# Kernel tuning notes

Measured on AMD Instinct MI355X. Metric: run time of the kernel, lower is better.

## Reference

```python
import jax, jax.numpy as jnp
import numpy as np

D_MODEL = 512
NUM_HEADS = 8
HEAD_DIM = D_MODEL // NUM_HEADS
BATCH = 4
SEQ = 2048
ROPE_BASE = 10000.0


def rope_cos_sin(seq_len, head_dim):
    inv_freq = 1.0 / (ROPE_BASE ** (jnp.arange(0, head_dim, 2, dtype=jnp.float32) / head_dim))
    t = jnp.arange(seq_len, dtype=jnp.float32)
    freqs = jnp.outer(t, inv_freq)              # (S, head_dim/2)
    emb = jnp.concatenate([freqs, freqs], axis=-1)  # (S, head_dim)
    return jnp.cos(emb), jnp.sin(emb)


def apply_rope(x, cos, sin):
    # x: (..., S, head_dim); cos/sin: (S, head_dim)
    x1 = x[..., ::2]
    x2 = x[..., 1::2]
    ch = cos[..., ::2]
    sh = sin[..., ::2]
    r1 = x1 * ch - x2 * sh
    r2 = x1 * sh + x2 * ch
    return jnp.stack([r1, r2], axis=-1).reshape(x.shape)


def setup_inputs() -> dict:
    key = jax.random.key(0)
    ks = jax.random.split(key, 12)
    x = jax.random.normal(ks[0], (BATCH, SEQ, D_MODEL), dtype=jnp.float32)
    variate_ids = jnp.sort(jax.random.randint(ks[1], (BATCH, SEQ), 0, 8), axis=-1).astype(jnp.int64)
    mask = jnp.ones((BATCH, SEQ), dtype=jnp.float32)
    s = 1.0 / np.sqrt(D_MODEL)
    Wq = jax.random.normal(ks[2], (D_MODEL, D_MODEL), dtype=jnp.float32) * s
    bq = jnp.zeros((D_MODEL,), dtype=jnp.float32)
    Wk = jax.random.normal(ks[3], (D_MODEL, D_MODEL), dtype=jnp.float32) * s
    bk = jnp.zeros((D_MODEL,), dtype=jnp.float32)
    Wv = jax.random.normal(ks[4], (D_MODEL, D_MODEL), dtype=jnp.float32) * s
    bv = jnp.zeros((D_MODEL,), dtype=jnp.float32)
    Wo = jax.random.normal(ks[5], (D_MODEL, D_MODEL), dtype=jnp.float32) * s
    bo = jnp.zeros((D_MODEL,), dtype=jnp.float32)
    u_same = jax.random.normal(ks[6], (NUM_HEADS,), dtype=jnp.float32) * 0.1
    u_cross = jax.random.normal(ks[7], (NUM_HEADS,), dtype=jnp.float32) * 0.1
    return dict(x=x, variate_ids=variate_ids, mask=mask, Wq=Wq, bq=bq, Wk=Wk, bk=bk,
                Wv=Wv, bv=bv, Wo=Wo, bo=bo, u_same=u_same, u_cross=u_cross)


def reference(x, variate_ids, mask, Wq, bq, Wk, bk, Wv, bv, Wo, bo, u_same, u_cross):
    B, S, D = x.shape
    H, Hd = NUM_HEADS, HEAD_DIM
    scale = 1.0 / np.sqrt(Hd)

    def proj(W, b):
        return (x @ W.T + b).reshape(B, S, H, Hd).transpose(0, 2, 1, 3)  # (B,H,S,Hd)

    q = proj(Wq, bq)
    k = proj(Wk, bk)
    v = proj(Wv, bv)

    cos, sin = rope_cos_sin(S, Hd)
    q = apply_rope(q, cos, sin)
    k = apply_rope(k, cos, sin)

    scores = jnp.einsum('bhid,bhjd->bhij', q, k) * scale  # (B,H,S,S)
    same = (variate_ids[:, :, None] == variate_ids[:, None, :]).astype(jnp.float32)  # (B,S,S)
    bias = same[:, None] * u_same[None, :, None, None] + (1.0 - same)[:, None] * u_cross[None, :, None, None]
    scores = scores + bias
    scores = scores + (1.0 - mask[:, None, None, :]) * -1e9
    probs = jax.nn.softmax(scores, axis=-1)
    out = jnp.einsum('bhij,bhjd->bhid', probs, v)  # (B,H,S,Hd)
    out = out.transpose(0, 2, 1, 3).reshape(B, S, D)
    return out @ Wo.T + bo
```

## Files before the change

### kernel.cpp

```cpp
#include <hip/hip_runtime.h>
#include <hip/hip_bf16.h>

#define BATCH   4
#define SEQ     2048
#define DMODEL  512
#define NHEADS  8
#define HEADDIM 64
#define MTOT    (BATCH*SEQ)
#define NX      (MTOT*DMODEL)
#define NW      (DMODEL*DMODEL)
#define QTILE   128
#define KTILE   64
#define NKT     (SEQ/KTILE)

#define LOG2E   1.4426950408889634f
#define SCL2    0.18033688011112042f
#define SHIFT   14.426950408889634f

typedef unsigned short u16;
typedef __bf16 bf16x8 __attribute__((ext_vector_type(8)));
typedef float  f32x4  __attribute__((ext_vector_type(4)));
typedef unsigned short u16x4 __attribute__((ext_vector_type(4)));
typedef unsigned u32x2 __attribute__((ext_vector_type(2)));

#define MFMA(a,b,c) __builtin_amdgcn_mfma_f32_16x16x32_bf16(a,b,c,0,0,0)

__device__ __forceinline__ u16 f2bf(float f) {
    unsigned u = __float_as_uint(f);
    u += 0x7FFFu + ((u >> 16) & 1u);
    return (u16)(u >> 16);
}

__device__ __forceinline__ unsigned pk_bf16(float a, float b) {
    union { __hip_bfloat162 h; unsigned u; } cv;
    cv.h = __float22bfloat162_rn(make_float2(a, b));
    return cv.u;
}

__device__ __forceinline__ float qsum16(float v) {
    v += __shfl_xor(v, 1);
    v += __shfl_xor(v, 2);
    v += __shfl_xor(v, 4);
    v += __shfl_xor(v, 8);
    return v;
}

__device__ __forceinline__ void gll16(const void* g, void* l) {
    __builtin_amdgcn_global_load_lds((const __attribute__((address_space(1))) void*)g,
                                     (__attribute__((address_space(3))) void*)l, 16, 0, 0);
}
__device__ __forceinline__ void gll4(const void* g, void* l) {
    __builtin_amdgcn_global_load_lds((const __attribute__((address_space(1))) void*)g,
                                     (__attribute__((address_space(3))) void*)l, 4, 0, 0);
}

#define NCVT4 ((NX + 4*NW)/4)
__global__ __launch_bounds__(256) void cvt_rope_kernel(
    const float* __restrict__ x,
    const float* __restrict__ wq, const float* __restrict__ wk,
    const float* __restrict__ wv, const float* __restrict__ wo,
    u16* __restrict__ xbf,
    u16* __restrict__ wqbf, u16* __restrict__ wkbf,
    u16* __restrict__ wvbf, u16* __restrict__ wobf,
    float2* __restrict__ cst)
{
    int i4 = blockIdx.x * 256 + threadIdx.x;
    if (i4 < NCVT4) {
        int i = i4 * 4;
        const float* s; u16* d; int o;
        if (i < NX) { s = x; d = xbf; o = i; }
        else {
            int j = i - NX;
            int r = j >> 18;
            o = j & (NW - 1);
            s = (r == 0) ? wq : (r == 1) ? wk : (r == 2) ? wv : wo;
            d = (r == 0) ? wqbf : (r == 1) ? wkbf : (r == 2) ? wvbf : wobf;
        }
        float4 v = *(const float4*)(s + o);
        u16x4 u = { f2bf(v.x), f2bf(v.y), f2bf(v.z), f2bf(v.w) };
        *(u16x4*)(d + o) = u;
    } else {
        int r = i4 - NCVT4;
        if (r < SEQ * 32 / 4) {
            int idx = r * 4;
            int s  = idx >> 5;
            int p0 = idx & 31;
#pragma unroll
            for (int t = 0; t < 4; ++t) {
                int p = p0 + t;
                float inv = __expf(-0.5756462732485115f * (float)(p & 15));
                float ang = (float)s * inv;
                cst[idx + t] = make_float2(cosf(ang), sinf(ang));
            }
        }
    }
}

__global__ __launch_bounds__(256) void qkv_kernel(
    const u16* __restrict__ x,
    const u16* __restrict__ Wq, const float* __restrict__ bq,
    const u16* __restrict__ Wk, const float* __restrict__ bk,
    const u16* __restrict__ Wv, const float* __restrict__ bv,
    const float2* __restrict__ cst,
    u16* __restrict__ qws, u16* __restrict__ kws, u16* __restrict__ vtws)
{
    __shared__ alignas(16) u16 As[128 * 64];
    __shared__ alignas(16) u16 Bs[128 * 64];

    const int m0 = blockIdx.x * 128;
    const int n0 = blockIdx.y * 128;
    const int tid  = threadIdx.x;
    const int w    = tid >> 6;
    const int lane = tid & 63;
    const int quad = lane >> 4;
    const int l16  = lane & 15;
    const int wm = w & 1, wn = w >> 1;

    const int sec = n0 >> 9;
    const int oc0 = n0 & 511;
    const u16*   Wm = (sec == 0) ? Wq : (sec == 1 ? Wk : Wv);
    const float* bb = (sec == 0) ? bq : (sec == 1 ? bk : bv);
    const float  sgn = (l16 & 1) ? 1.0f : -1.0f;

    f32x4 acc[4][4] = {};

    for (int kb = 0; kb < 8; ++kb) {
#pragma unroll
        for (int it = 0; it < 4; ++it) {
            const int s   = it * 256 + tid;
            const int row = s >> 3;
            const int cb  = s & 7;
            const int gcol = kb * 64 + (((cb ^ (row & 7))) << 3);
            gll16(x  + (m0  + row) * 512 + gcol, &As[s * 8]);
            gll16(Wm + (oc0 + row) * 512 + gcol, &Bs[s * 8]);
        }
        __syncthreads();

#pragma unroll
        for (int ks = 0; ks < 2; ++ks) {
            bf16x8 a[4], bfr[4];
#pragma unroll
            for (int t = 0; t < 4; ++t) {
                const int arow = wm * 64 + t * 16 + l16;
                a[t]   = *(const bf16x8*)&As[arow * 64 + (((ks * 4 + quad) ^ (arow & 7)) << 3)];
                const int brow = wn * 64 + t * 16 + l16;
                bfr[t] = *(const bf16x8*)&Bs[brow * 64 + (((ks * 4 + quad) ^ (brow & 7)) << 3)];
            }
#pragma unroll
            for (int tm = 0; tm < 4; ++tm)
#pragma unroll
                for (int tn = 0; tn < 4; ++tn)
                    acc[tm][tn] = MFMA(a[tm], bfr[tn], acc[tm][tn]);
        }
        __syncthreads();
    }

#pragma unroll
    for (int tm = 0; tm < 4; ++tm) {
        const int R0 = m0 + wm * 64 + tm * 16 + quad * 4;
        const int bi = R0 >> 11;
        const int s0 = R0 & 2047;
#pragma unroll
        for (int tn = 0; tn < 4; ++tn) {
            const int col = oc0 + wn * 64 + tn * 16 + l16;
            const int hh  = col >> 6;
            const int d   = col & 63;
            const float bval = bb[col];
            const size_t hb = (size_t)(bi * NHEADS + hh) * (SEQ * HEADDIM);
            float res[4];
            if (sec < 2) {
#pragma unroll
                for (int r = 0; r < 4; ++r) {
                    float val = acc[tm][tn][r] + bval;
                    float other = __shfl_xor(val, 1);
                    float2 cs = cst[(s0 + r) * 32 + (d >> 1)];
                    res[r] = fmaf(val, cs.x, other * (sgn * cs.y));
                }
                const unsigned p01 = pk_bf16(res[0], res[1]);
                const unsigned p23 = pk_bf16(res[2], res[3]);
                u16* dp = ((sec == 0) ? qws : kws) + hb + (size_t)s0 * HEADDIM + d;
                dp[0]   = (u16)p01;  dp[64]  = (u16)(p01 >> 16);
                dp[128] = (u16)p23;  dp[192] = (u16)(p23 >> 16);
            } else {
#pragma unroll
                for (int r = 0; r < 4; ++r) res[r] = acc[tm][tn][r] + bval;
                u32x2 pv = { pk_bf16(res[0], res[1]), pk_bf16(res[2], res[3]) };
                *(u32x2*)(vtws + hb + (size_t)d * SEQ + s0) = pv;
            }
        }
    }
}

__global__ __launch_bounds__(512, 4) void attn_kernel(
    const u16* __restrict__ qws, const u16* __restrict__ kws,
    const u16* __restrict__ vtl,
    const int* __restrict__ vids, const float* __restrict__ mask,
    const float* __restrict__ u_same, const float* __restrict__ u_cross,
    u16* __restrict__ attn)
{
    __shared__ alignas(16) u16 kbuf[2][KTILE * 64];
    __shared__ alignas(16) u16 vbuf[2][KTILE * 64];
    __shared__ alignas(16) u16 pls[8][16][72];
    __shared__ int   bid[2][KTILE];
    __shared__ float bmk[2][KTILE];

    const int bh = blockIdx.y;
    const int b  = bh >> 3;
    const int h  = bh & 7;
    const int q0 = blockIdx.x * QTILE;

    const int tid  = threadIdx.x;
    const int w    = tid >> 6;
    const int lane = tid & 63;
    const int quad = lane >> 4;
    const int l16  = lane & 15;

    const float us2 = u_same[h]  * LOG2E;
    const float uc2 = u_cross[h] * LOG2E;
    const size_t tb = (size_t)bh * (SEQ * HEADDIM);

    const int qr = q0 + w * 16 + l16;
    const bf16x8 aq0 = *(const bf16x8*)(qws + tb + qr * HEADDIM + quad * 8);
    const bf16x8 aq1 = *(const bf16x8*)(qws + tb + qr * HEADDIM + 32 + quad * 8);

    int vq[4];
#pragma unroll
    for (int r = 0; r < 4; ++r)
        vq[r] = vids[b * SEQ + q0 + w * 16 + quad * 4 + r];

    float li[4] = {0.f, 0.f, 0.f, 0.f};
    f32x4 o[4] = {};

    const int srow = w * 8 + (lane >> 3);
    const int scb  = lane & 7;
    const int soff = ((scb ^ (srow & 7)) << 3);
    auto stage = [&](int kt, int nb) {
        const int k0 = kt * KTILE;
        gll16(kws + tb + (size_t)(k0 + srow) * HEADDIM + soff, &kbuf[nb][w * 512 + (lane & 7) * 8 + ((lane >> 3) & 7) * 0 + lane * 8 - lane * 8 + (srow - w * 8) * 64 + scb * 8]);
        gll16(vtl + tb + (size_t)srow * SEQ + k0 + soff,        &vbuf[nb][(srow - w * 8) * 64 + w * 512 + scb * 8]);
        if (w == 0) {
            gll4(vids + b * SEQ + k0 + lane, &bid[nb][0]);
            gll4(mask + b * SEQ + k0 + lane, &bmk[nb][0]);
        }
    };

    auto body = [&](const int cur) {
#pragma unroll
        for (int nt = 0; nt < 4; ++nt) {
            const int krow = nt * 16 + l16;
            const int r7   = krow & 7;
            const bf16x8 kb0 = *(const bf16x8*)&kbuf[cur][krow * 64 + ((quad ^ r7) << 3)];
            const bf16x8 kb1 = *(const bf16x8*)&kbuf[cur][krow * 64 + ((quad ^ r7 ^ 4) << 3)];
            f32x4 sc = {};
            sc = MFMA(aq0, kb0, sc);
            sc = MFMA(aq1, kb1, sc);
            const int   kv  = bid[cur][krow];
            const float mdl = fmaf(bmk[cur][krow], 1.4426950408889634e9f,
                                   -1.4426950408889634e9f - SHIFT);
            const float as_ = us2 + mdl;
            const float ac_ = uc2 + mdl;
            float p[4];
#pragma unroll
            for (int r = 0; r < 4; ++r) {
                const float sel = (kv == vq[r]) ? as_ : ac_;
                p[r] = exp2f(fmaf(sc[r], SCL2, sel));
                li[r] += p[r];
            }
            const unsigned p01 = pk_bf16(p[0], p[1]);
            const unsigned p23 = pk_bf16(p[2], p[3]);
            u16* pb = &pls[w][quad * 4][nt * 16 + l16];
            pb[0]       = (u16)p01;  pb[72]      = (u16)(p01 >> 16);
            pb[2 * 72]  = (u16)p23;  pb[3 * 72]  = (u16)(p23 >> 16);
        }

        const bf16x8 ap0 = *(const bf16x8*)&pls[w][l16][quad * 8];
        const bf16x8 ap1 = *(const bf16x8*)&pls[w][l16][32 + quad * 8];

#pragma unroll
        for (int nt = 0; nt < 4; ++nt) {
            const int vrow = nt * 16 + l16;
            const int r7   = vrow & 7;
            const bf16x8 vb0 = *(const bf16x8*)&vbuf[cur][vrow * 64 + ((quad ^ r7) << 3)];
            const bf16x8 vb1 = *(const bf16x8*)&vbuf[cur][vrow * 64 + ((quad ^ r7 ^ 4) << 3)];
            o[nt] = MFMA(ap0, vb0, o[nt]);
            o[nt] = MFMA(ap1, vb1, o[nt]);
        }
    };

    stage(0, 0);
    for (int kt = 0; kt < NKT; kt += 2) {
        __syncthreads();
        stage(kt + 1, 1);
        body(0);
        __syncthreads();
        if (kt + 2 < NKT) stage(kt + 2, 0);
        body(1);
    }

#pragma unroll
    for (int r = 0; r < 4; ++r) {
        const float inv = 1.0f / qsum16(li[r]);
        const int R = q0 + w * 16 + quad * 4 + r;
        const int rb = (b * SEQ + R) * DMODEL + h * HEADDIM;
#pragma unroll
        for (int nt = 0; nt < 4; ++nt)
            attn[rb + nt * 16 + l16] = f2bf(o[nt][r] * inv);
    }
}

__global__ __launch_bounds__(256) void proj_kernel(
    const u16* __restrict__ a, const u16* __restrict__ Wo,
    const float* __restrict__ bo, float* __restrict__ out)
{
    __shared__ alignas(16) u16 As[128 * 64];
    __shared__ alignas(16) u16 Bs[128 * 64];

    const int m0 = blockIdx.x * 128;
    const int n0 = blockIdx.y * 128;
    const int tid  = threadIdx.x;
    const int w    = tid >> 6;
    const int lane = tid & 63;
    const int quad = lane >> 4;
    const int l16  = lane & 15;
    const int wm = w & 1, wn = w >> 1;

    f32x4 acc[4][4] = {};

    for (int kb = 0; kb < 8; ++kb) {
#pragma unroll
        for (int it = 0; it < 4; ++it) {
            const int s   = it * 256 + tid;
            const int row = s >> 3;
            const int cb  = s & 7;
            const int gcol = kb * 64 + (((cb ^ (row & 7))) << 3);
            gll16(a  + (m0 + row) * 512 + gcol, &As[s * 8]);
            gll16(Wo + (n0 + row) * 512 + gcol, &Bs[s * 8]);
        }
        __syncthreads();

#pragma unroll
        for (int ks = 0; ks < 2; ++ks) {
            bf16x8 av[4], bv[4];
#pragma unroll
            for (int t = 0; t < 4; ++t) {
                const int arow = wm * 64 + t * 16 + l16;
                av[t] = *(const bf16x8*)&As[arow * 64 + (((ks * 4 + quad) ^ (arow & 7)) << 3)];
                const int brow = wn * 64 + t * 16 + l16;
                bv[t] = *(const bf16x8*)&Bs[brow * 64 + (((ks * 4 + quad) ^ (brow & 7)) << 3)];
            }
#pragma unroll
            for (int tm = 0; tm < 4; ++tm)
#pragma unroll
                for (int tn = 0; tn < 4; ++tn)
                    acc[tm][tn] = MFMA(av[tm], bv[tn], acc[tm][tn]);
        }
        __syncthreads();
    }

#pragma unroll
    for (int tm = 0; tm < 4; ++tm) {
#pragma unroll
        for (int tn = 0; tn < 4; ++tn) {
            const int col = n0 + wn * 64 + tn * 16 + l16;
            const float bval = bo[col];
#pragma unroll
            for (int r = 0; r < 4; ++r) {
                const int R = m0 + wm * 64 + tm * 16 + quad * 4 + r;
                out[R * 512 + col] = acc[tm][tn][r] + bval;
            }
        }
    }
}

extern "C" void kernel_launch(void* const* d_in, const int* in_sizes, int n_in,
                              void* d_out, int out_size, void* d_ws, size_t ws_size,
                              hipStream_t stream) {
    const float* x    = (const float*)d_in[0];
    const int*   vids = (const int*)d_in[1];
    const float* mask = (const float*)d_in[2];
    const float* Wq = (const float*)d_in[3];
    const float* bq = (const float*)d_in[4];
    const float* Wk = (const float*)d_in[5];
    const float* bk = (const float*)d_in[6];
    const float* Wv = (const float*)d_in[7];
    const float* bv = (const float*)d_in[8];
    const float* Wo = (const float*)d_in[9];
    const float* bo = (const float*)d_in[10];
    const float* usame  = (const float*)d_in[11];
    const float* ucross = (const float*)d_in[12];
    float* out = (float*)d_out;

    u16* xbf  = (u16*)d_ws;
    u16* wqbf = xbf + NX;
    u16* wkbf = wqbf + NW;
    u16* wvbf = wkbf + NW;
    u16* wobf = wvbf + NW;
    float2* cst = (float2*)(wobf + NW);
    u16* qws  = (u16*)(cst + SEQ * 32);
    u16* kws  = qws + (size_t)BATCH * NHEADS * SEQ * HEADDIM;
    u16* vtws = kws + (size_t)BATCH * NHEADS * SEQ * HEADDIM;
    u16* attn = xbf;

    cvt_rope_kernel<<<(NCVT4 + SEQ * 32 / 4 + 255) / 256, 256, 0, stream>>>(
        x, Wq, Wk, Wv, Wo, xbf, wqbf, wkbf, wvbf, wobf, cst);

    dim3 g1(MTOT / 128, 3 * DMODEL / 128);
    qkv_kernel<<<g1, 256, 0, stream>>>(xbf, wqbf, bq, wkbf, bk, wvbf, bv,
                                       cst, qws, kws, vtws);

    dim3 g2(SEQ / QTILE, BATCH * NHEADS);
    attn_kernel<<<g2, 512, 0, stream>>>(qws, kws, vtws, vids, mask,
                                        usame, ucross, attn);

    dim3 g3(MTOT / 128, DMODEL / 128);
    proj_kernel<<<g3, 256, 0, stream>>>(attn, wobf, bo, out);
}
```

Baseline: 207.1 us.

## Process two query subtiles per attention wave and stage V transpose through LDS

The attention kernel moves from 512 to 256 threads per block, with each wave now handling two 16-row query subtiles. K and V fragments read from shared memory are reused across both subtiles, which halves LDS reads per MFMA, at the cost of more registers per thread. Separately, the QKV kernel's V epilogue now writes the transposed tile into padded shared memory and then emits coalesced 16-byte global stores, replacing the scattered 8-byte transposed stores.

```diff
diff --git a/kernel.cpp b/kernel.cpp
--- a/kernel.cpp
+++ b/kernel.cpp
@@ -96,6 +96,7 @@
     }
 }
 
+#define TP 136
 __global__ __launch_bounds__(256) void qkv_kernel(
     const u16* __restrict__ x,
     const u16* __restrict__ Wq, const float* __restrict__ bq,
@@ -104,8 +105,9 @@
     const float2* __restrict__ cst,
     u16* __restrict__ qws, u16* __restrict__ kws, u16* __restrict__ vtws)
 {
-    __shared__ alignas(16) u16 As[128 * 64];
-    __shared__ alignas(16) u16 Bs[128 * 64];
+    __shared__ alignas(16) u16 smem[128 * TP];
+    u16* As = smem;
+    u16* Bs = smem + 8192;
 
     const int m0 = blockIdx.x * 128;
     const int n0 = blockIdx.y * 128;
@@ -155,20 +157,20 @@
         __syncthreads();
     }
 
-#pragma unroll
-    for (int tm = 0; tm < 4; ++tm) {
-        const int R0 = m0 + wm * 64 + tm * 16 + quad * 4;
-        const int bi = R0 >> 11;
-        const int s0 = R0 & 2047;
-#pragma unroll
-        for (int tn = 0; tn < 4; ++tn) {
-            const int col = oc0 + wn * 64 + tn * 16 + l16;
-            const int hh  = col >> 6;
-            const int d   = col & 63;
-            const float bval = bb[col];
-            const size_t hb = (size_t)(bi * NHEADS + hh) * (SEQ * HEADDIM);
-            float res[4];
-            if (sec < 2) {
+    if (sec < 2) {
+#pragma unroll
+        for (int tm = 0; tm < 4; ++tm) {
+            const int R0 = m0 + wm * 64 + tm * 16 + quad * 4;
+            const int bi = R0 >> 11;
+            const int s0 = R0 & 2047;
+#pragma unroll
+            for (int tn = 0; tn < 4; ++tn) {
+                const int col = oc0 + wn * 64 + tn * 16 + l16;
+                const int hh  = col >> 6;
+                const int d   = col & 63;
+                const float bval = bb[col];
+                const size_t hb = (size_t)(bi * NHEADS + hh) * (SEQ * HEADDIM);
+                float res[4];
 #pragma unroll
                 for (int r = 0; r < 4; ++r) {
                     float val = acc[tm][tn][r] + bval;
@@ -181,17 +183,40 @@
                 u16* dp = ((sec == 0) ? qws : kws) + hb + (size_t)s0 * HEADDIM + d;
                 dp[0]   = (u16)p01;  dp[64]  = (u16)(p01 >> 16);
                 dp[128] = (u16)p23;  dp[192] = (u16)(p23 >> 16);
-            } else {
-#pragma unroll
-                for (int r = 0; r < 4; ++r) res[r] = acc[tm][tn][r] + bval;
-                u32x2 pv = { pk_bf16(res[0], res[1]), pk_bf16(res[2], res[3]) };
-                *(u32x2*)(vtws + hb + (size_t)d * SEQ + s0) = pv;
-            }
-        }
-    }
-}
-
-__global__ __launch_bounds__(512, 4) void attn_kernel(
+            }
+        }
+    } else {
+#pragma unroll
+        for (int tm = 0; tm < 4; ++tm) {
+            const int row_l = wm * 64 + tm * 16 + quad * 4;
+#pragma unroll
+            for (int tn = 0; tn < 4; ++tn) {
+                const int col_l = wn * 64 + tn * 16 + l16;
+                const float bval = bb[oc0 + col_l];
+                u32x2 pv = { pk_bf16(acc[tm][tn][0] + bval, acc[tm][tn][1] + bval),
+                             pk_bf16(acc[tm][tn][2] + bval, acc[tm][tn][3] + bval) };
+                *(u32x2*)&smem[col_l * TP + row_l] = pv;
+            }
+        }
+        __syncthreads();
+        const int bi  = m0 >> 11;
+        const int sgb = m0 & 2047;
+#pragma unroll
+        for (int i = 0; i < 8; ++i) {
+            const int c    = i * 256 + tid;
+            const int col  = c >> 4;
+            const int sc8  = (c & 15) * 8;
+            const int gcol = oc0 + col;
+            const int hh   = gcol >> 6;
+            const int d    = gcol & 63;
+            u16* dst = vtws + (size_t)(bi * NHEADS + hh) * (SEQ * HEADDIM)
+                            + (size_t)d * SEQ + sgb + sc8;
+            *(bf16x8*)dst = *(const bf16x8*)&smem[col * TP + sc8];
+        }
+    }
+}
+
+__global__ __launch_bounds__(256) void attn_kernel(
     const u16* __restrict__ qws, const u16* __restrict__ kws,
     const u16* __restrict__ vtl,
     const int* __restrict__ vids, const float* __restrict__ mask,
@@ -200,7 +225,7 @@
 {
     __shared__ alignas(16) u16 kbuf[2][KTILE * 64];
     __shared__ alignas(16) u16 vbuf[2][KTILE * 64];
-    __shared__ alignas(16) u16 pls[8][16][72];
+    __shared__ alignas(16) u16 pls[4][32][72];
     __shared__ int   bid[2][KTILE];
     __shared__ float bmk[2][KTILE];
 
@@ -219,25 +244,34 @@
     const float uc2 = u_cross[h] * LOG2E;
     const size_t tb = (size_t)bh * (SEQ * HEADDIM);
 
-    const int qr = q0 + w * 16 + l16;
-    const bf16x8 aq0 = *(const bf16x8*)(qws + tb + qr * HEADDIM + quad * 8);
-    const bf16x8 aq1 = *(const bf16x8*)(qws + tb + qr * HEADDIM + 32 + quad * 8);
-
-    int vq[4];
-#pragma unroll
-    for (int r = 0; r < 4; ++r)
-        vq[r] = vids[b * SEQ + q0 + w * 16 + quad * 4 + r];
-
-    float li[4] = {0.f, 0.f, 0.f, 0.f};
-    f32x4 o[4] = {};
-
-    const int srow = w * 8 + (lane >> 3);
-    const int scb  = lane & 7;
-    const int soff = ((scb ^ (srow & 7)) << 3);
+    bf16x8 aq[2][2];
+#pragma unroll
+    for (int s = 0; s < 2; ++s) {
+        const int qr = q0 + s * 64 + w * 16 + l16;
+        aq[s][0] = *(const bf16x8*)(qws + tb + qr * HEADDIM + quad * 8);
+        aq[s][1] = *(const bf16x8*)(qws + tb + qr * HEADDIM + 32 + quad * 8);
+    }
+    int vq[2][4];
+#pragma unroll
+    for (int s = 0; s < 2; ++s)
+#pragma unroll
+        for (int r = 0; r < 4; ++r)
+            vq[s][r] = vids[b * SEQ + q0 + s * 64 + w * 16 + quad * 4 + r];
+
+    float li[2][4] = {};
+    f32x4 o[2][4] = {};
+
     auto stage = [&](int kt, int nb) {
         const int k0 = kt * KTILE;
-        gll16(kws + tb + (size_t)(k0 + srow) * HEADDIM + soff, &kbuf[nb][w * 512 + (lane & 7) * 8 + ((lane >> 3) & 7) * 0 + lane * 8 - lane * 8 + (srow - w * 8) * 64 + scb * 8]);
-        gll16(vtl + tb + (size_t)srow * SEQ + k0 + soff,        &vbuf[nb][(srow - w * 8) * 64 + w * 512 + scb * 8]);
+#pragma unroll
+        for (int i = 0; i < 2; ++i) {
+            const int srow = w * 16 + i * 8 + (lane >> 3);
+            const int scb  = lane & 7;
+            const int soff = ((scb ^ (srow & 7)) << 3);
+            const int doff = srow * 64 + scb * 8;
+            gll16(kws + tb + (size_t)(k0 + srow) * HEADDIM + soff, &kbuf[nb][doff]);
+            gll16(vtl + tb + (size_t)srow * SEQ + k0 + soff,       &vbuf[nb][doff]);
+        }
         if (w == 0) {
             gll4(vids + b * SEQ + k0 + lane, &bid[nb][0]);
             gll4(mask + b * SEQ + k0 + lane, &bmk[nb][0]);
@@ -251,30 +285,37 @@
             const int r7   = krow & 7;
             const bf16x8 kb0 = *(const bf16x8*)&kbuf[cur][krow * 64 + ((quad ^ r7) << 3)];
             const bf16x8 kb1 = *(const bf16x8*)&kbuf[cur][krow * 64 + ((quad ^ r7 ^ 4) << 3)];
-            f32x4 sc = {};
-            sc = MFMA(aq0, kb0, sc);
-            sc = MFMA(aq1, kb1, sc);
             const int   kv  = bid[cur][krow];
             const float mdl = fmaf(bmk[cur][krow], 1.4426950408889634e9f,
                                    -1.4426950408889634e9f - SHIFT);
             const float as_ = us2 + mdl;
             const float ac_ = uc2 + mdl;
-            float p[4];
-#pragma unroll
-            for (int r = 0; r < 4; ++r) {
-                const float sel = (kv == vq[r]) ? as_ : ac_;
-                p[r] = exp2f(fmaf(sc[r], SCL2, sel));
-                li[r] += p[r];
-            }
-            const unsigned p01 = pk_bf16(p[0], p[1]);
-            const unsigned p23 = pk_bf16(p[2], p[3]);
-            u16* pb = &pls[w][quad * 4][nt * 16 + l16];
-            pb[0]       = (u16)p01;  pb[72]      = (u16)(p01 >> 16);
-            pb[2 * 72]  = (u16)p23;  pb[3 * 72]  = (u16)(p23 >> 16);
-        }
-
-        const bf16x8 ap0 = *(const bf16x8*)&pls[w][l16][quad * 8];
-        const bf16x8 ap1 = *(const bf16x8*)&pls[w][l16][32 + quad * 8];
+#pragma unroll
+            for (int s = 0; s < 2; ++s) {
+                f32x4 sc = {};
+                sc = MFMA(aq[s][0], kb0, sc);
+                sc = MFMA(aq[s][1], kb1, sc);
+                float p[4];
+#pragma unroll
+                for (int r = 0; r < 4; ++r) {
+                    const float sel = (kv == vq[s][r]) ? as_ : ac_;
+                    p[r] = exp2f(fmaf(sc[r], SCL2, sel));
+                    li[s][r] += p[r];
+                }
+                const unsigned p01 = pk_bf16(p[0], p[1]);
+                const unsigned p23 = pk_bf16(p[2], p[3]);
+                u16* pb = &pls[w][s * 16 + quad * 4][nt * 16 + l16];
+                pb[0]      = (u16)p01;  pb[72]     = (u16)(p01 >> 16);
+                pb[2 * 72] = (u16)p23;  pb[3 * 72] = (u16)(p23 >> 16);
+            }
+        }
+
+        bf16x8 ap[2][2];
+#pragma unroll
+        for (int s = 0; s < 2; ++s) {
+            ap[s][0] = *(const bf16x8*)&pls[w][s * 16 + l16][quad * 8];
+            ap[s][1] = *(const bf16x8*)&pls[w][s * 16 + l16][32 + quad * 8];
+        }
 
 #pragma unroll
         for (int nt = 0; nt < 4; ++nt) {
@@ -282,8 +323,11 @@
             const int r7   = vrow & 7;
             const bf16x8 vb0 = *(const bf16x8*)&vbuf[cur][vrow * 64 + ((quad ^ r7) << 3)];
             const bf16x8 vb1 = *(const bf16x8*)&vbuf[cur][vrow * 64 + ((quad ^ r7 ^ 4) << 3)];
-            o[nt] = MFMA(ap0, vb0, o[nt]);
-            o[nt] = MFMA(ap1, vb1, o[nt]);
+#pragma unroll
+            for (int s = 0; s < 2; ++s) {
+                o[s][nt] = MFMA(ap[s][0], vb0, o[s][nt]);
+                o[s][nt] = MFMA(ap[s][1], vb1, o[s][nt]);
+            }
         }
     };
 
@@ -298,14 +342,16 @@
     }
 
 #pragma unroll
-    for (int r = 0; r < 4; ++r) {
-        const float inv = 1.0f / qsum16(li[r]);
-        const int R = q0 + w * 16 + quad * 4 + r;
-        const int rb = (b * SEQ + R) * DMODEL + h * HEADDIM;
-#pragma unroll
-        for (int nt = 0; nt < 4; ++nt)
-            attn[rb + nt * 16 + l16] = f2bf(o[nt][r] * inv);
-    }
+    for (int s = 0; s < 2; ++s)
+#pragma unroll
+        for (int r = 0; r < 4; ++r) {
+            const float inv = 1.0f / qsum16(li[s][r]);
+            const int R = q0 + s * 64 + w * 16 + quad * 4 + r;
+            const int rb = (b * SEQ + R) * DMODEL + h * HEADDIM;
+#pragma unroll
+            for (int nt = 0; nt < 4; ++nt)
+                attn[rb + nt * 16 + l16] = f2bf(o[s][nt][r] * inv);
+        }
 }
 
 __global__ __launch_bounds__(256) void proj_kernel(
@@ -409,7 +455,7 @@
                                        cst, qws, kws, vtws);
 
     dim3 g2(SEQ / QTILE, BATCH * NHEADS);
-    attn_kernel<<<g2, 512, 0, stream>>>(qws, kws, vtws, vids, mask,
+    attn_kernel<<<g2, 256, 0, stream>>>(qws, kws, vtws, vids, mask,
                                         usame, ucross, attn);
 
     dim3 g3(MTOT / 128, DMODEL / 128);
```

Measured after the change: 215.2 us. 3.9% more time.

## Stage GEMM epilogues through LDS for coalesced 16-byte global stores

Applied to the files above, without the earlier changes.

The QKV and output-projection GEMM epilogues now transpose their accumulator tiles into padded shared memory, then write to global memory with wide coalesced vector stores. This replaces the scattered 2-byte and 4-byte writes. For Q/K the MFMA operand order is swapped so each lane holds consecutive head-dim elements, which lets RoPE pairs be rotated in-register without shuffles. The cost is extra LDS traffic and barriers, and the output projection now runs its epilogue in two halves.

```diff
diff --git a/kernel.cpp b/kernel.cpp
--- a/kernel.cpp
+++ b/kernel.cpp
@@ -30,13 +30,11 @@
     u += 0x7FFFu + ((u >> 16) & 1u);
     return (u16)(u >> 16);
 }
-
 __device__ __forceinline__ unsigned pk_bf16(float a, float b) {
     union { __hip_bfloat162 h; unsigned u; } cv;
     cv.h = __float22bfloat162_rn(make_float2(a, b));
     return cv.u;
 }
-
 __device__ __forceinline__ float qsum16(float v) {
     v += __shfl_xor(v, 1);
     v += __shfl_xor(v, 2);
@@ -44,7 +42,6 @@
     v += __shfl_xor(v, 8);
     return v;
 }
-
 __device__ __forceinline__ void gll16(const void* g, void* l) {
     __builtin_amdgcn_global_load_lds((const __attribute__((address_space(1))) void*)g,
                                      (__attribute__((address_space(3))) void*)l, 16, 0, 0);
@@ -96,16 +93,18 @@
     }
 }
 
+#define TP 136
 __global__ __launch_bounds__(256) void qkv_kernel(
     const u16* __restrict__ x,
     const u16* __restrict__ Wq, const float* __restrict__ bq,
     const u16* __restrict__ Wk, const float* __restrict__ bk,
     const u16* __restrict__ Wv, const float* __restrict__ bv,
-    const float2* __restrict__ cst,
+    const float* __restrict__ cstf,
     u16* __restrict__ qws, u16* __restrict__ kws, u16* __restrict__ vtws)
 {
-    __shared__ alignas(16) u16 As[128 * 64];
-    __shared__ alignas(16) u16 Bs[128 * 64];
+    __shared__ alignas(16) u16 smem[128 * TP];
+    u16* As = smem;
+    u16* Bs = smem + 8192;
 
     const int m0 = blockIdx.x * 128;
     const int n0 = blockIdx.y * 128;
@@ -120,7 +119,9 @@
     const int oc0 = n0 & 511;
     const u16*   Wm = (sec == 0) ? Wq : (sec == 1 ? Wk : Wv);
     const float* bb = (sec == 0) ? bq : (sec == 1 ? bk : bv);
-    const float  sgn = (l16 & 1) ? 1.0f : -1.0f;
+
+    const int xb = (sec < 2) ? wn : wm;
+    const int wb = (sec < 2) ? wm : wn;
 
     f32x4 acc[4][4] = {};
 
@@ -138,55 +139,98 @@
 
 #pragma unroll
         for (int ks = 0; ks < 2; ++ks) {
-            bf16x8 a[4], bfr[4];
+            bf16x8 xf[4], wf[4];
 #pragma unroll
             for (int t = 0; t < 4; ++t) {
-                const int arow = wm * 64 + t * 16 + l16;
-                a[t]   = *(const bf16x8*)&As[arow * 64 + (((ks * 4 + quad) ^ (arow & 7)) << 3)];
-                const int brow = wn * 64 + t * 16 + l16;
-                bfr[t] = *(const bf16x8*)&Bs[brow * 64 + (((ks * 4 + quad) ^ (brow & 7)) << 3)];
-            }
-#pragma unroll
-            for (int tm = 0; tm < 4; ++tm)
-#pragma unroll
-                for (int tn = 0; tn < 4; ++tn)
-                    acc[tm][tn] = MFMA(a[tm], bfr[tn], acc[tm][tn]);
-        }
-        __syncthreads();
-    }
-
-#pragma unroll
-    for (int tm = 0; tm < 4; ++tm) {
-        const int R0 = m0 + wm * 64 + tm * 16 + quad * 4;
-        const int bi = R0 >> 11;
-        const int s0 = R0 & 2047;
-#pragma unroll
-        for (int tn = 0; tn < 4; ++tn) {
-            const int col = oc0 + wn * 64 + tn * 16 + l16;
-            const int hh  = col >> 6;
-            const int d   = col & 63;
-            const float bval = bb[col];
-            const size_t hb = (size_t)(bi * NHEADS + hh) * (SEQ * HEADDIM);
-            float res[4];
+                const int xrow = xb * 64 + t * 16 + l16;
+                const int wrow = wb * 64 + t * 16 + l16;
+                xf[t] = *(const bf16x8*)&As[xrow * 64 + (((ks * 4 + quad) ^ (xrow & 7)) << 3)];
+                wf[t] = *(const bf16x8*)&Bs[wrow * 64 + (((ks * 4 + quad) ^ (wrow & 7)) << 3)];
+            }
             if (sec < 2) {
 #pragma unroll
-                for (int r = 0; r < 4; ++r) {
-                    float val = acc[tm][tn][r] + bval;
-                    float other = __shfl_xor(val, 1);
-                    float2 cs = cst[(s0 + r) * 32 + (d >> 1)];
-                    res[r] = fmaf(val, cs.x, other * (sgn * cs.y));
-                }
-                const unsigned p01 = pk_bf16(res[0], res[1]);
-                const unsigned p23 = pk_bf16(res[2], res[3]);
-                u16* dp = ((sec == 0) ? qws : kws) + hb + (size_t)s0 * HEADDIM + d;
-                dp[0]   = (u16)p01;  dp[64]  = (u16)(p01 >> 16);
-                dp[128] = (u16)p23;  dp[192] = (u16)(p23 >> 16);
+                for (int tm = 0; tm < 4; ++tm)
+#pragma unroll
+                    for (int tn = 0; tn < 4; ++tn)
+                        acc[tm][tn] = MFMA(wf[tm], xf[tn], acc[tm][tn]);
             } else {
 #pragma unroll
-                for (int r = 0; r < 4; ++r) res[r] = acc[tm][tn][r] + bval;
-                u32x2 pv = { pk_bf16(res[0], res[1]), pk_bf16(res[2], res[3]) };
-                *(u32x2*)(vtws + hb + (size_t)d * SEQ + s0) = pv;
-            }
+                for (int tm = 0; tm < 4; ++tm)
+#pragma unroll
+                    for (int tn = 0; tn < 4; ++tn)
+                        acc[tm][tn] = MFMA(xf[tm], wf[tn], acc[tm][tn]);
+            }
+        }
+        __syncthreads();
+    }
+
+    if (sec < 2) {
+#pragma unroll
+        for (int tm = 0; tm < 4; ++tm) {
+            const int dls = wm * 64 + tm * 16 + quad * 4;
+            const float4 bv4 = *(const float4*)&bb[oc0 + dls];
+            const int pbase = ((oc0 + dls) & 63) >> 1;
+#pragma unroll
+            for (int tn = 0; tn < 4; ++tn) {
+                const int sl = wn * 64 + tn * 16 + l16;
+                const int sg = (m0 + sl) & 2047;
+                const float4 cs = *(const float4*)&cstf[sg * 64 + pbase * 2];
+                const float v0 = acc[tm][tn][0] + bv4.x;
+                const float v1 = acc[tm][tn][1] + bv4.y;
+                const float v2 = acc[tm][tn][2] + bv4.z;
+                const float v3 = acc[tm][tn][3] + bv4.w;
+                const float r0 = v0 * cs.x - v1 * cs.y;
+                const float r1 = v1 * cs.x + v0 * cs.y;
+                const float r2 = v2 * cs.z - v3 * cs.w;
+                const float r3 = v3 * cs.z + v2 * cs.w;
+                u32x2 pv = { pk_bf16(r0, r1), pk_bf16(r2, r3) };
+                *(u32x2*)&smem[sl * TP + dls] = pv;
+            }
+        }
+        __syncthreads();
+        u16* dst0 = (sec == 0) ? qws : kws;
+#pragma unroll
+        for (int i = 0; i < 8; ++i) {
+            const int c   = i * 256 + tid;
+            const int sl  = c >> 4;
+            const int d8  = (c & 15) * 8;
+            const int gcol = oc0 + d8;
+            const int hh  = gcol >> 6;
+            const int dh  = gcol & 63;
+            const int sgl = m0 + sl;
+            const int bi  = sgl >> 11;
+            const int s   = sgl & 2047;
+            u16* dst = dst0 + (size_t)(bi * NHEADS + hh) * (SEQ * HEADDIM)
+                            + (size_t)s * HEADDIM + dh;
+            *(bf16x8*)dst = *(const bf16x8*)&smem[sl * TP + d8];
+        }
+    } else {
+#pragma unroll
+        for (int tm = 0; tm < 4; ++tm) {
+            const int row_l = wm * 64 + tm * 16 + quad * 4;
+#pragma unroll
+            for (int tn = 0; tn < 4; ++tn) {
+                const int col_l = wn * 64 + tn * 16 + l16;
+                const float bval = bb[oc0 + col_l];
+                u32x2 pv = { pk_bf16(acc[tm][tn][0] + bval, acc[tm][tn][1] + bval),
+                             pk_bf16(acc[tm][tn][2] + bval, acc[tm][tn][3] + bval) };
+                *(u32x2*)&smem[col_l * TP + row_l] = pv;
+            }
+        }
+        __syncthreads();
+        const int bi  = m0 >> 11;
+        const int sgb = m0 & 2047;
+#pragma unroll
+        for (int i = 0; i < 8; ++i) {
+            const int c    = i * 256 + tid;
+            const int col  = c >> 4;
+            const int sc8  = (c & 15) * 8;
+            const int gcol = oc0 + col;
+            const int hh   = gcol >> 6;
+            const int d    = gcol & 63;
+            u16* dst = vtws + (size_t)(bi * NHEADS + hh) * (SEQ * HEADDIM)
+                            + (size_t)d * SEQ + sgb + sc8;
+            *(bf16x8*)dst = *(const bf16x8*)&smem[col * TP + sc8];
         }
     }
 }
@@ -236,8 +280,8 @@
     const int soff = ((scb ^ (srow & 7)) << 3);
     auto stage = [&](int kt, int nb) {
         const int k0 = kt * KTILE;
-        gll16(kws + tb + (size_t)(k0 + srow) * HEADDIM + soff, &kbuf[nb][w * 512 + (lane & 7) * 8 + ((lane >> 3) & 7) * 0 + lane * 8 - lane * 8 + (srow - w * 8) * 64 + scb * 8]);
-        gll16(vtl + tb + (size_t)srow * SEQ + k0 + soff,        &vbuf[nb][(srow - w * 8) * 64 + w * 512 + scb * 8]);
+        gll16(kws + tb + (size_t)(k0 + srow) * HEADDIM + soff, &kbuf[nb][w * 512 + lane * 8]);
+        gll16(vtl + tb + (size_t)srow * SEQ + k0 + soff,       &vbuf[nb][w * 512 + lane * 8]);
         if (w == 0) {
             gll4(vids + b * SEQ + k0 + lane, &bid[nb][0]);
             gll4(mask + b * SEQ + k0 + lane, &bmk[nb][0]);
@@ -312,8 +356,10 @@
     const u16* __restrict__ a, const u16* __restrict__ Wo,
     const float* __restrict__ bo, float* __restrict__ out)
 {
-    __shared__ alignas(16) u16 As[128 * 64];
-    __shared__ alignas(16) u16 Bs[128 * 64];
+    __shared__ alignas(16) u16 psm[132 * 64 * 2];
+    u16* As = psm;
+    u16* Bs = psm + 8192;
+    float* Lp = (float*)psm;
 
     const int m0 = blockIdx.x * 128;
     const int n0 = blockIdx.y * 128;
@@ -340,35 +386,49 @@
 
 #pragma unroll
         for (int ks = 0; ks < 2; ++ks) {
-            bf16x8 av[4], bv[4];
+            bf16x8 af[4], wf[4];
 #pragma unroll
             for (int t = 0; t < 4; ++t) {
-                const int arow = wm * 64 + t * 16 + l16;
-                av[t] = *(const bf16x8*)&As[arow * 64 + (((ks * 4 + quad) ^ (arow & 7)) << 3)];
-                const int brow = wn * 64 + t * 16 + l16;
-                bv[t] = *(const bf16x8*)&Bs[brow * 64 + (((ks * 4 + quad) ^ (brow & 7)) << 3)];
+                const int arow = wn * 64 + t * 16 + l16;
+                const int wrow = wm * 64 + t * 16 + l16;
+                af[t] = *(const bf16x8*)&As[arow * 64 + (((ks * 4 + quad) ^ (arow & 7)) << 3)];
+                wf[t] = *(const bf16x8*)&Bs[wrow * 64 + (((ks * 4 + quad) ^ (wrow & 7)) << 3)];
             }
 #pragma unroll
             for (int tm = 0; tm < 4; ++tm)
 #pragma unroll
                 for (int tn = 0; tn < 4; ++tn)
-                    acc[tm][tn] = MFMA(av[tm], bv[tn], acc[tm][tn]);
-        }
-        __syncthreads();
-    }
-
-#pragma unroll
-    for (int tm = 0; tm < 4; ++tm) {
-#pragma unroll
-        for (int tn = 0; tn < 4; ++tn) {
-            const int col = n0 + wn * 64 + tn * 16 + l16;
-            const float bval = bo[col];
-#pragma unroll
-            for (int r = 0; r < 4; ++r) {
-                const int R = m0 + wm * 64 + tm * 16 + quad * 4 + r;
-                out[R * 512 + col] = acc[tm][tn][r] + bval;
-            }
-        }
+                    acc[tm][tn] = MFMA(wf[tm], af[tn], acc[tm][tn]);
+        }
+        __syncthreads();
+    }
+
+#pragma unroll
+    for (int hph = 0; hph < 2; ++hph) {
+        if (wn == hph) {
+#pragma unroll
+            for (int tm = 0; tm < 4; ++tm) {
+                const int dls = wm * 64 + tm * 16 + quad * 4;
+                const float4 bv4 = *(const float4*)&bo[n0 + dls];
+#pragma unroll
+                for (int tn = 0; tn < 4; ++tn) {
+                    const int s2 = tn * 16 + l16;
+                    float4 v = { acc[tm][tn][0] + bv4.x, acc[tm][tn][1] + bv4.y,
+                                 acc[tm][tn][2] + bv4.z, acc[tm][tn][3] + bv4.w };
+                    *(float4*)&Lp[s2 * 132 + dls] = v;
+                }
+            }
+        }
+        __syncthreads();
+#pragma unroll
+        for (int i = 0; i < 8; ++i) {
+            const int c  = i * 256 + tid;
+            const int s2 = c >> 5;
+            const int dq = (c & 31) * 4;
+            float4 v = *(const float4*)&Lp[s2 * 132 + dq];
+            *(float4*)&out[(size_t)(m0 + hph * 64 + s2) * 512 + n0 + dq] = v;
+        }
+        __syncthreads();
     }
 }
 
@@ -406,7 +466,7 @@
 
     dim3 g1(MTOT / 128, 3 * DMODEL / 128);
     qkv_kernel<<<g1, 256, 0, stream>>>(xbf, wqbf, bq, wkbf, bk, wvbf, bv,
-                                       cst, qws, kws, vtws);
+                                       (const float*)cst, qws, kws, vtws);
 
     dim3 g2(SEQ / QTILE, BATCH * NHEADS);
     attn_kernel<<<g2, 512, 0, stream>>>(qws, kws, vtws, vids, mask,
```

Result: no change. 204.8 us (-1.1%).
